# Optimization experiments

Hardware: AMD Instinct MI355X
Metric: run time of the kernel (lower is better)

## Reference

```python
import jax, jax.numpy as jnp
import numpy as np

M = 4096
N = 4096

def _twiddle(L):
    k = jnp.arange(L, dtype=jnp.float32)
    ang = -np.pi * k / (2.0 * L)
    return jnp.stack([jnp.cos(ang), jnp.sin(ang)], axis=-1).astype(jnp.float32)  # [L,2] = exp(-i*pi*k/(2L))

def setup_inputs() -> dict:
    key = jax.random.key(0)
    x = jax.random.normal(key, (M, N), dtype=jnp.float32)
    return {"x": x, "expkM": _twiddle(M), "expkN": _twiddle(N)}

def reference(x, expkM, expkN):
    # 2D DCT-II via Makhoul even/odd reordering + single complex FFT2 + twiddle multiply.
    # out[u,v] = sum_{m,n} x[m,n] cos(pi*u*(2m+1)/(2M)) cos(pi*v*(2n+1)/(2N))
    Mh, Nh = x.shape
    permM = jnp.concatenate([jnp.arange(0, Mh, 2), jnp.arange(Mh - 1, 0, -2)])
    permN = jnp.concatenate([jnp.arange(0, Nh, 2), jnp.arange(Nh - 1, 0, -2)])
    y = x[permM][:, permN]                       # even/odd reorder in both dims
    Y = jnp.fft.fft2(y)                          # [M,N] complex
    wM = expkM[:, 0] + 1j * expkM[:, 1]          # exp(-i*pi*u/(2M))
    wN = expkN[:, 0] + 1j * expkN[:, 1]          # exp(-i*pi*v/(2N))
    Yrev = jnp.roll(Y[::-1, :], 1, axis=0)       # Y[(M-u) % M, v]
    C = 0.5 * (wN[None, :] * Y + jnp.conj(wN)[None, :] * jnp.conj(Yrev))
    return jnp.real(wM[:, None] * C)
```

## Files before the change

kernel.cpp:

```cpp
#include <hip/hip_runtime.h>
#include <math.h>

#define NFULL 4096
#define NH    2048
#define T     256

__device__ __forceinline__ int pad(int i) { return i + (i >> 3); }

__device__ __forceinline__ float2 cmul(float2 a, float2 b) {
    return make_float2(a.x * b.x - a.y * b.y, a.x * b.y + a.y * b.x);
}

__device__ __forceinline__ void dft8(float2 v[8]) {
    const float s = 0.70710678118654752f;
    float2 e0 = v[0], o0 = v[1], e1 = v[2], o1 = v[3];
    float2 e2 = v[4], o2 = v[5], e3 = v[6], o3 = v[7];
    float2 t0 = make_float2(e0.x + e2.x, e0.y + e2.y);
    float2 t1 = make_float2(e0.x - e2.x, e0.y - e2.y);
    float2 t2 = make_float2(e1.x + e3.x, e1.y + e3.y);
    float2 t3 = make_float2(e1.x - e3.x, e1.y - e3.y);
    float2 E0 = make_float2(t0.x + t2.x, t0.y + t2.y);
    float2 E2 = make_float2(t0.x - t2.x, t0.y - t2.y);
    float2 E1 = make_float2(t1.x + t3.y, t1.y - t3.x);
    float2 E3 = make_float2(t1.x - t3.y, t1.y + t3.x);
    float2 u0 = make_float2(o0.x + o2.x, o0.y + o2.y);
    float2 u1 = make_float2(o0.x - o2.x, o0.y - o2.y);
    float2 u2 = make_float2(o1.x + o3.x, o1.y + o3.y);
    float2 u3 = make_float2(o1.x - o3.x, o1.y - o3.y);
    float2 O0 = make_float2(u0.x + u2.x, u0.y + u2.y);
    float2 O2 = make_float2(u0.x - u2.x, u0.y - u2.y);
    float2 O1 = make_float2(u1.x + u3.y, u1.y - u3.x);
    float2 O3 = make_float2(u1.x - u3.y, u1.y + u3.x);
    O1 = make_float2(s * (O1.x + O1.y), s * (O1.y - O1.x));
    O2 = make_float2(O2.y, -O2.x);
    O3 = make_float2(s * (O3.y - O3.x), s * (-O3.x - O3.y));
    v[0] = make_float2(E0.x + O0.x, E0.y + O0.y);
    v[4] = make_float2(E0.x - O0.x, E0.y - O0.y);
    v[1] = make_float2(E1.x + O1.x, E1.y + O1.y);
    v[5] = make_float2(E1.x - O1.x, E1.y - O1.y);
    v[2] = make_float2(E2.x + O2.x, E2.y + O2.y);
    v[6] = make_float2(E2.x - O2.x, E2.y - O2.y);
    v[3] = make_float2(E3.x + O3.x, E3.y + O3.y);
    v[7] = make_float2(E3.x - O3.x, E3.y - O3.y);
}

__device__ __forceinline__ void dft4(float2 v[4]) {
    float2 t0 = make_float2(v[0].x + v[2].x, v[0].y + v[2].y);
    float2 t1 = make_float2(v[0].x - v[2].x, v[0].y - v[2].y);
    float2 t2 = make_float2(v[1].x + v[3].x, v[1].y + v[3].y);
    float2 t3 = make_float2(v[1].x - v[3].x, v[1].y - v[3].y);
    v[0] = make_float2(t0.x + t2.x, t0.y + t2.y);
    v[2] = make_float2(t0.x - t2.x, t0.y - t2.y);
    v[1] = make_float2(t1.x + t3.y, t1.y - t3.x);
    v[3] = make_float2(t1.x - t3.y, t1.y + t3.x);
}

__global__ __launch_bounds__(T) void dct_rows_rfft(const float* __restrict__ in,
                                                   const float* __restrict__ expk,
                                                   float* __restrict__ out) {
    __shared__ float2 A[NH + (NH >> 3)];
    __shared__ float2 B[NH + (NH >> 3)];
    const int row = blockIdx.x;
    const int t = threadIdx.x;
    const float4* __restrict__ src4 = (const float4*)(in + (size_t)row * NFULL);

    #pragma unroll
    for (int i = 0; i < 4; ++i) {
        int c = t + T * i;
        float4 f = src4[c];
        A[pad(c)]        = make_float2(f.x, f.z);
        A[pad(2047 - c)] = make_float2(f.w, f.y);
    }
    __syncthreads();

    float2 v[8];
    {
        const int j = t;
        #pragma unroll
        for (int r = 0; r < 8; ++r) v[r] = A[pad(j + 256 * r)];
        dft8(v);
        #pragma unroll
        for (int r = 0; r < 8; ++r) B[pad(8 * j + r)] = v[r];
    }
    __syncthreads();
    {
        const int j = t;
        #pragma unroll
        for (int r = 0; r < 8; ++r) v[r] = B[pad(j + 256 * r)];
        float ang = -2.0f * (float)M_PI * (float)(j & 7) / 64.0f;
        float sn, cs;
        __sincosf(ang, &sn, &cs);
        float2 w1 = make_float2(cs, sn), w = w1;
        v[1] = cmul(v[1], w);
        #pragma unroll
        for (int r = 2; r < 8; ++r) { w = cmul(w, w1); v[r] = cmul(v[r], w); }
        dft8(v);
        const int d = ((j >> 3) << 6) + (j & 7);
        #pragma unroll
        for (int r = 0; r < 8; ++r) A[pad(d + 8 * r)] = v[r];
    }
    __syncthreads();
    {
        const int j = t;
        #pragma unroll
        for (int r = 0; r < 8; ++r) v[r] = A[pad(j + 256 * r)];
        float ang = -2.0f * (float)M_PI * (float)(j & 63) / 512.0f;
        float sn, cs;
        __sincosf(ang, &sn, &cs);
        float2 w1 = make_float2(cs, sn), w = w1;
        v[1] = cmul(v[1], w);
        #pragma unroll
        for (int r = 2; r < 8; ++r) { w = cmul(w, w1); v[r] = cmul(v[r], w); }
        dft8(v);
        const int d = ((j >> 6) << 9) + (j & 63);
        #pragma unroll
        for (int r = 0; r < 8; ++r) B[pad(d + 64 * r)] = v[r];
    }
    __syncthreads();
    #pragma unroll
    for (int h = 0; h < 2; ++h) {
        const int j = t + 256 * h;
        float2 u[4];
        #pragma unroll
        for (int r = 0; r < 4; ++r) u[r] = B[pad(j + 512 * r)];
        float ang = -2.0f * (float)M_PI * (float)j / 2048.0f;
        float sn, cs;
        __sincosf(ang, &sn, &cs);
        float2 w1 = make_float2(cs, sn);
        u[1] = cmul(u[1], w1);
        float2 w2 = cmul(w1, w1);
        u[2] = cmul(u[2], w2);
        u[3] = cmul(u[3], cmul(w2, w1));
        dft4(u);
        #pragma unroll
        for (int r = 0; r < 4; ++r) A[pad(j + 512 * r)] = u[r];
    }
    __syncthreads();

    const float2* __restrict__ ek = (const float2*)expk;
    float* __restrict__ dst = out + (size_t)row * NFULL;
    #pragma unroll
    for (int i = 0; i < 8; ++i) {
        const int k = t + T * i;
        if (k == 0) {
            float2 z0 = A[pad(0)];
            dst[0]    = ek[0].x * (z0.x + z0.y);
            dst[NH]   = ek[NH].x * (z0.x - z0.y);
        } else {
            float2 Zk = A[pad(k)];
            float2 Zr = A[pad(NH - k)];
            float2 E = make_float2(0.5f * (Zk.x + Zr.x), 0.5f * (Zk.y - Zr.y));
            float2 O = make_float2(0.5f * (Zk.y + Zr.y), 0.5f * (Zr.x - Zk.x));
            float2 wk = ek[k];
            float2 w2 = cmul(wk, wk);
            float2 uu = cmul(w2, w2);
            float2 Y = make_float2(E.x + uu.x * O.x - uu.y * O.y,
                                   E.y + uu.x * O.y + uu.y * O.x);
            dst[k] = wk.x * Y.x - wk.y * Y.y;
            float2 wn = ek[NFULL - k];
            dst[NFULL - k] = wn.x * Y.x + wn.y * Y.y;
        }
    }
}

__global__ __launch_bounds__(256) void transpose4k(const float* __restrict__ in,
                                                   float* __restrict__ out) {
    __shared__ float tile[32][33];
    const int x0 = blockIdx.x * 32;
    const int y0 = blockIdx.y * 32;
    const int tx = threadIdx.x & 31;
    const int ty = threadIdx.x >> 5;

    #pragma unroll
    for (int i = 0; i < 32; i += 8)
        tile[ty + i][tx] = in[(size_t)(y0 + ty + i) * NFULL + (x0 + tx)];
    __syncthreads();
    #pragma unroll
    for (int i = 0; i < 32; i += 8)
        out[(size_t)(x0 + ty + i) * NFULL + (y0 + tx)] = tile[tx][ty + i];
}

extern "C" void kernel_launch(void* const* d_in, const int* in_sizes, int n_in,
                              void* d_out, int out_size, void* d_ws, size_t ws_size,
                              hipStream_t stream) {
    const float* x     = (const float*)d_in[0];
    const float* expkM = (const float*)d_in[1];
    const float* expkN = (const float*)d_in[2];
    float* out = (float*)d_out;
    float* ws1 = (float*)d_ws;

    dct_rows_rfft<<<NFULL, T, 0, stream>>>(x, expkN, ws1);
    transpose4k<<<dim3(128, 128), 256, 0, stream>>>(ws1, out);
    dct_rows_rfft<<<NFULL, T, 0, stream>>>(out, expkM, ws1);
    transpose4k<<<dim3(128, 128), 256, 0, stream>>>(ws1, out);
}
```

Before: 102.4 us.

## Use single LDS buffer and precomputed twiddle table in row DCT kernel

Drops the second shared-memory ping-pong buffer and does every FFT stage in place in one array, with extra barriers between the reads and the writes. This halves LDS use per block and adds launch_bounds(256,6) to raise occupancy. Per-thread sincos and twiddle-power chains are replaced by loads from a 4096-entry twiddle table that a small extra kernel fills each call. The trade-offs are more barriers, scattered global (L2-resident) twiddle loads, and one more kernel launch.

```diff
diff --git a/kernel.cpp b/kernel.cpp
--- a/kernel.cpp
+++ b/kernel.cpp
@@ -55,11 +55,19 @@
     v[3] = make_float2(t1.x - t3.y, t1.y + t3.x);
 }
 
-__global__ __launch_bounds__(T) void dct_rows_rfft(const float* __restrict__ in,
-                                                   const float* __restrict__ expk,
-                                                   float* __restrict__ out) {
+__global__ __launch_bounds__(256) void init_tw(float2* __restrict__ tw) {
+    int k = blockIdx.x * 256 + threadIdx.x;
+    float ang = -2.0f * (float)M_PI * (float)k / 4096.0f;
+    float s, c;
+    sincosf(ang, &s, &c);
+    tw[k] = make_float2(c, s);
+}
+
+__global__ __launch_bounds__(T, 6) void dct_rows_rfft(const float* __restrict__ in,
+                                                      const float* __restrict__ expk,
+                                                      const float2* __restrict__ tw,
+                                                      float* __restrict__ out) {
     __shared__ float2 A[NH + (NH >> 3)];
-    __shared__ float2 B[NH + (NH >> 3)];
     const int row = blockIdx.x;
     const int t = threadIdx.x;
     const float4* __restrict__ src4 = (const float4*)(in + (size_t)row * NFULL);
@@ -78,59 +86,58 @@
         const int j = t;
         #pragma unroll
         for (int r = 0; r < 8; ++r) v[r] = A[pad(j + 256 * r)];
+        __syncthreads();
         dft8(v);
         #pragma unroll
-        for (int r = 0; r < 8; ++r) B[pad(8 * j + r)] = v[r];
-    }
-    __syncthreads();
+        for (int r = 0; r < 8; ++r) A[pad(8 * j + r)] = v[r];
+        __syncthreads();
+    }
     {
         const int j = t;
-        #pragma unroll
-        for (int r = 0; r < 8; ++r) v[r] = B[pad(j + 256 * r)];
-        float ang = -2.0f * (float)M_PI * (float)(j & 7) / 64.0f;
-        float sn, cs;
-        __sincosf(ang, &sn, &cs);
-        float2 w1 = make_float2(cs, sn), w = w1;
-        v[1] = cmul(v[1], w);
-        #pragma unroll
-        for (int r = 2; r < 8; ++r) { w = cmul(w, w1); v[r] = cmul(v[r], w); }
+        const int m = 64 * (j & 7);
+        #pragma unroll
+        for (int r = 0; r < 8; ++r) v[r] = A[pad(j + 256 * r)];
+        float2 w1 = tw[m], w2 = tw[2 * m], w3 = tw[3 * m];
+        float2 w4 = tw[4 * m], w5 = tw[5 * m], w6 = tw[6 * m], w7 = tw[7 * m];
+        __syncthreads();
+        v[1] = cmul(v[1], w1); v[2] = cmul(v[2], w2); v[3] = cmul(v[3], w3);
+        v[4] = cmul(v[4], w4); v[5] = cmul(v[5], w5); v[6] = cmul(v[6], w6);
+        v[7] = cmul(v[7], w7);
         dft8(v);
         const int d = ((j >> 3) << 6) + (j & 7);
         #pragma unroll
         for (int r = 0; r < 8; ++r) A[pad(d + 8 * r)] = v[r];
-    }
-    __syncthreads();
+        __syncthreads();
+    }
     {
         const int j = t;
+        const int m = 8 * (j & 63);
         #pragma unroll
         for (int r = 0; r < 8; ++r) v[r] = A[pad(j + 256 * r)];
-        float ang = -2.0f * (float)M_PI * (float)(j & 63) / 512.0f;
-        float sn, cs;
-        __sincosf(ang, &sn, &cs);
-        float2 w1 = make_float2(cs, sn), w = w1;
-        v[1] = cmul(v[1], w);
-        #pragma unroll
-        for (int r = 2; r < 8; ++r) { w = cmul(w, w1); v[r] = cmul(v[r], w); }
+        float2 w1 = tw[m], w2 = tw[2 * m], w3 = tw[3 * m];
+        float2 w4 = tw[4 * m], w5 = tw[5 * m], w6 = tw[6 * m], w7 = tw[7 * m];
+        __syncthreads();
+        v[1] = cmul(v[1], w1); v[2] = cmul(v[2], w2); v[3] = cmul(v[3], w3);
+        v[4] = cmul(v[4], w4); v[5] = cmul(v[5], w5); v[6] = cmul(v[6], w6);
+        v[7] = cmul(v[7], w7);
         dft8(v);
         const int d = ((j >> 6) << 9) + (j & 63);
         #pragma unroll
-        for (int r = 0; r < 8; ++r) B[pad(d + 64 * r)] = v[r];
-    }
-    __syncthreads();
+        for (int r = 0; r < 8; ++r) A[pad(d + 64 * r)] = v[r];
+        __syncthreads();
+    }
     #pragma unroll
     for (int h = 0; h < 2; ++h) {
         const int j = t + 256 * h;
         float2 u[4];
         #pragma unroll
-        for (int r = 0; r < 4; ++r) u[r] = B[pad(j + 512 * r)];
-        float ang = -2.0f * (float)M_PI * (float)j / 2048.0f;
-        float sn, cs;
-        __sincosf(ang, &sn, &cs);
-        float2 w1 = make_float2(cs, sn);
+        for (int r = 0; r < 4; ++r) u[r] = A[pad(j + 512 * r)];
+        float2 w1 = tw[2 * j];
+        float2 w2 = tw[4 * j];
+        float2 w3 = tw[(6 * j) & 4095];
         u[1] = cmul(u[1], w1);
-        float2 w2 = cmul(w1, w1);
         u[2] = cmul(u[2], w2);
-        u[3] = cmul(u[3], cmul(w2, w1));
+        u[3] = cmul(u[3], w3);
         dft4(u);
         #pragma unroll
         for (int r = 0; r < 4; ++r) A[pad(j + 512 * r)] = u[r];
@@ -144,18 +151,17 @@
         const int k = t + T * i;
         if (k == 0) {
             float2 z0 = A[pad(0)];
-            dst[0]    = ek[0].x * (z0.x + z0.y);
-            dst[NH]   = ek[NH].x * (z0.x - z0.y);
+            dst[0]  = ek[0].x * (z0.x + z0.y);
+            dst[NH] = ek[NH].x * (z0.x - z0.y);
         } else {
             float2 Zk = A[pad(k)];
             float2 Zr = A[pad(NH - k)];
             float2 E = make_float2(0.5f * (Zk.x + Zr.x), 0.5f * (Zk.y - Zr.y));
             float2 O = make_float2(0.5f * (Zk.y + Zr.y), 0.5f * (Zr.x - Zk.x));
-            float2 wk = ek[k];
-            float2 w2 = cmul(wk, wk);
-            float2 uu = cmul(w2, w2);
+            float2 uu = tw[k];
             float2 Y = make_float2(E.x + uu.x * O.x - uu.y * O.y,
                                    E.y + uu.x * O.y + uu.y * O.x);
+            float2 wk = ek[k];
             dst[k] = wk.x * Y.x - wk.y * Y.y;
             float2 wn = ek[NFULL - k];
             dst[NFULL - k] = wn.x * Y.x + wn.y * Y.y;
@@ -188,9 +194,11 @@
     const float* expkN = (const float*)d_in[2];
     float* out = (float*)d_out;
     float* ws1 = (float*)d_ws;
-
-    dct_rows_rfft<<<NFULL, T, 0, stream>>>(x, expkN, ws1);
+    float2* tw = (float2*)((char*)d_ws + (size_t)NFULL * NFULL * 4);
+
+    init_tw<<<16, 256, 0, stream>>>(tw);
+    dct_rows_rfft<<<NFULL, T, 0, stream>>>(x, expkN, tw, ws1);
     transpose4k<<<dim3(128, 128), 256, 0, stream>>>(ws1, out);
-    dct_rows_rfft<<<NFULL, T, 0, stream>>>(out, expkM, ws1);
+    dct_rows_rfft<<<NFULL, T, 0, stream>>>(out, expkM, tw, ws1);
     transpose4k<<<dim3(128, 128), 256, 0, stream>>>(ws1, out);
 }
```

After: 150.6 us. 47.0% more time.
